# Kernel tuning notes

Measured on AMD Instinct MI355X. Metric: run time of the kernel, lower is better.

## Reference

```python
import jax, jax.numpy as jnp
import numpy as np

B, S, D, H = 2, 2048, 768, 12
DK = D // H
NEG = -10000.0


def setup_inputs() -> dict:
    key = jax.random.key(0)
    ks = jax.random.split(key, 12)
    def lin(k):
        kw, kb = jax.random.split(k)
        return (jax.random.normal(kw, (D, D), jnp.float32) * 0.02,
                jax.random.normal(kb, (D,), jnp.float32) * 0.02)
    Wq, bq = lin(ks[0]); Wk, bk = lin(ks[1]); Wv, bv = lin(ks[2]); Wo, bo = lin(ks[3])
    query = jax.random.normal(ks[4], (B, S, D), jnp.float32)
    key_t = jax.random.normal(ks[5], (B, S, D), jnp.float32)
    value = jax.random.normal(ks[6], (B, S, D), jnp.float32)
    # causal mask, broadcastable to [B,H,S,S]; positions with 0 are masked
    mask = jnp.tril(jnp.ones((S, S), jnp.int32))[None, None, :, :]
    return {"query": query, "key": key_t, "value": value, "mask": mask,
            "Wq": Wq, "bq": bq, "Wk": Wk, "bk": bk, "Wv": Wv, "bv": bv,
            "Wo": Wo, "bo": bo}


def reference(query, key, value, mask, Wq, bq, Wk, bk, Wv, bv, Wo, bo):
    # torch.nn.Linear: y = x @ W^T + b
    def split_heads(x):  # [B,S,D] -> [B,H,S,DK]
        return x.reshape(B, S, H, DK).transpose(0, 2, 1, 3)
    q = split_heads(query @ Wq.T + bq)
    k = split_heads(key @ Wk.T + bk)
    v = split_heads(value @ Wv.T + bv)
    scores = jnp.einsum('bhqd,bhkd->bhqk', q, k) / jnp.sqrt(jnp.float32(DK))
    scores = jnp.where(mask == 0, NEG, scores)  # masked_fill(mask==0, -1e4)
    attn = jax.nn.softmax(scores, axis=-1)      # dropout p=0.0 -> identity
    x = jnp.einsum('bhqk,bhkd->bhqd', attn, v)  # [B,H,S,DK]
    x = x.transpose(0, 2, 1, 3).reshape(B, S, D)
    return x @ Wo.T + bo
```

## Files before the change

### kernel.cpp

```cpp
#include <hip/hip_runtime.h>
#include <cstdint>


#define B_ 2
#define S_ 2048
#define D_ 768
#define H_ 12
#define DK_ 64

typedef __bf16 bf16;
typedef __bf16 bf16x8 __attribute__((ext_vector_type(8)));
typedef float f32x4 __attribute__((ext_vector_type(4)));
typedef uint32_t u32x4 __attribute__((ext_vector_type(4)));
typedef uint16_t u16x4 __attribute__((ext_vector_type(4)));

__device__ __forceinline__ f32x4 mfma16(bf16x8 a, bf16x8 b, f32x4 c) {
  return __builtin_amdgcn_mfma_f32_16x16x32_bf16(a, b, c, 0, 0, 0);
}

struct raw8 { u32x4 a, b; };

__device__ __forceinline__ raw8 fetch8(const void* base, size_t off, int isbf) {
  raw8 r;
  if (isbf) {
    r.a = *(const u32x4*)((const bf16*)base + off);
  } else {
    const float* f = (const float*)base + off;
    r.a = *(const u32x4*)f;
    r.b = *(const u32x4*)(f + 4);
  }
  return r;
}

__device__ __forceinline__ bf16x8 cvt8(raw8 r, int isbf) {
  if (isbf) return __builtin_bit_cast(bf16x8, r.a);
  const float4 x = __builtin_bit_cast(float4, r.a);
  const float4 y = __builtin_bit_cast(float4, r.b);
  bf16x8 o;
  o[0]=(bf16)x.x; o[1]=(bf16)x.y; o[2]=(bf16)x.z; o[3]=(bf16)x.w;
  o[4]=(bf16)y.x; o[5]=(bf16)y.y; o[6]=(bf16)y.z; o[7]=(bf16)y.w;
  return o;
}

__device__ __forceinline__ float load_scalar(const void* base, int idx, int isbf) {
  return isbf ? (float)((const bf16*)base)[idx] : ((const float*)base)[idx];
}

__device__ __forceinline__ uint32_t pack2bf(float lo, float hi) {
  const uint16_t l = __builtin_bit_cast(uint16_t, (bf16)lo);
  const uint16_t h = __builtin_bit_cast(uint16_t, (bf16)hi);
  return (uint32_t)l | ((uint32_t)h << 16);
}

__device__ __forceinline__ int sniff(const void* q) {
  __shared__ int cnt;
  if (threadIdx.x == 0) cnt = 0;
  __syncthreads();
  int local = 0;
  const uint32_t* qw = (const uint32_t*)q;
  for (int i = (int)threadIdx.x; i < 1024; i += 256) {
    const uint32_t e = (qw[i] >> 7) & 0xff;
    if (e >= 96 && e <= 140) local++;
  }
  atomicAdd(&cnt, local);
  __syncthreads();
  return (cnt >= 600) ? 1 : 0;
}

#define GEMM_CVT(Xg, xbf, Wg, wbf, m0, n0)                                   \
  __shared__ __align__(16) bf16 As[2][128][40];                              \
  __shared__ __align__(16) bf16 Bs[2][128][40];                              \
  const int t = (int)threadIdx.x;                                            \
  const int lane = t & 63, w = t >> 6, c = lane & 15, quad = lane >> 4;      \
  const int wm = w & 1, wn = w >> 1;                                         \
  const int srow = t >> 1, scol = (t & 1) * 16;                              \
  f32x4 acc[4][4];                                                           \
  _Pragma("unroll") for (int i = 0; i < 4; ++i)                              \
      _Pragma("unroll") for (int j = 0; j < 4; ++j)                          \
          _Pragma("unroll") for (int e = 0; e < 4; ++e) acc[i][j][e] = 0.0f; \
  raw8 pa[2], pb[2];                                                         \
  auto fetchAB = [&](int k0) {                                               \
    _Pragma("unroll") for (int u = 0; u < 2; ++u) {                          \
      pa[u] = fetch8(Xg, (size_t)(m0 + srow) * D_ + k0 + scol + u * 8, xbf); \
      pb[u] = fetch8(Wg, (size_t)(n0 + srow) * D_ + k0 + scol + u * 8, wbf); \
    }                                                                        \
  };                                                                         \
  fetchAB(0);                                                                \
  int p = 0;                                                                 \
  for (int kt = 0; kt < D_ / 32; ++kt) {                                     \
    _Pragma("unroll") for (int u = 0; u < 2; ++u) {                          \
      *(bf16x8*)&As[p][srow][scol + u * 8] = cvt8(pa[u], xbf);               \
      *(bf16x8*)&Bs[p][srow][scol + u * 8] = cvt8(pb[u], wbf);               \
    }                                                                        \
    __syncthreads();                                                         \
    if (kt + 1 < D_ / 32) fetchAB((kt + 1) * 32);                            \
    bf16x8 af[4], bfr[4];                                                    \
    _Pragma("unroll") for (int i = 0; i < 4; ++i) {                          \
      af[i] = *(const bf16x8*)&As[p][wm * 64 + i * 16 + c][quad * 8];        \
      bfr[i] = *(const bf16x8*)&Bs[p][wn * 64 + i * 16 + c][quad * 8];       \
    }                                                                        \
    _Pragma("unroll") for (int i = 0; i < 4; ++i)                            \
        _Pragma("unroll") for (int j = 0; j < 4; ++j)                        \
            acc[i][j] = mfma16(af[i], bfr[j], acc[i][j]);                    \
    p ^= 1;                                                                  \
  }

__global__ __launch_bounds__(256) void qkv_kernel(
    const void* __restrict__ q, const void* __restrict__ k,
    const void* __restrict__ v,
    const void* __restrict__ Wq, const void* __restrict__ Wk,
    const void* __restrict__ Wv,
    const void* __restrict__ bq, const void* __restrict__ bk,
    const void* __restrict__ bv,
    bf16* __restrict__ qh, bf16* __restrict__ kh, bf16* __restrict__ vt,
    int* __restrict__ flag)
{
  const int isbf = sniff(q);
  if (blockIdx.x == 0 && blockIdx.y == 0 && threadIdx.x == 0) *flag = isbf;
  const int z = (int)blockIdx.y / 6;
  const int n0 = ((int)blockIdx.y % 6) * 128;
  const int m0 = (int)blockIdx.x * 128;
  const void* Xg = (z == 0) ? q : (z == 1) ? k : v;
  const void* Wg = (z == 0) ? Wq : (z == 1) ? Wk : Wv;
  const void* bias = (z == 0) ? bq : (z == 1) ? bk : bv;
  bf16* out = (z == 0) ? qh : (z == 1) ? kh : vt;

  GEMM_CVT(Xg, isbf, Wg, isbf, m0, n0)

#pragma unroll
  for (int j = 0; j < 4; ++j) {
    const int n = n0 + wn * 64 + j * 16 + c;
    const int h = n >> 6, dk = n & 63;
    const float bv_ = load_scalar(bias, n, isbf);
    if (z != 2) {
#pragma unroll
      for (int i = 0; i < 4; ++i)
#pragma unroll
        for (int r = 0; r < 4; ++r) {
          const int m = m0 + wm * 64 + i * 16 + quad * 4 + r;
          const int bi = m >> 11, s = m & (S_ - 1);
          out[(((size_t)bi * H_ + h) * S_ + s) * DK_ + dk] =
              (bf16)(acc[i][j][r] + bv_);
        }
    } else {
#pragma unroll
      for (int i = 0; i < 4; ++i) {
        const int m = m0 + wm * 64 + i * 16 + quad * 4;
        const int bi = m >> 11, s0 = m & (S_ - 1);
        u16x4 pk;
#pragma unroll
        for (int r = 0; r < 4; ++r)
          pk[r] = __builtin_bit_cast(uint16_t, (bf16)(acc[i][j][r] + bv_));
        *(u16x4*)&out[(((size_t)bi * H_ + h) * DK_ + dk) * S_ + s0] = pk;
      }
    }
  }
}

__global__ __launch_bounds__(256) void oproj_kernel(
    const bf16* __restrict__ xh, const void* __restrict__ Wo,
    const void* __restrict__ bias, void* __restrict__ out,
    const int* __restrict__ flag)
{
  const int isbf = *flag;
  const int m0 = (int)blockIdx.x * 128;
  const int n0 = (int)blockIdx.y * 128;

  GEMM_CVT(xh, 1, Wo, isbf, m0, n0)

#pragma unroll
  for (int j = 0; j < 4; ++j) {
    const int n = n0 + wn * 64 + j * 16 + c;
    const float bv_ = load_scalar(bias, n, isbf);
#pragma unroll
    for (int i = 0; i < 4; ++i)
#pragma unroll
      for (int r = 0; r < 4; ++r) {
        const int m = m0 + wm * 64 + i * 16 + quad * 4 + r;
        const float v = acc[i][j][r] + bv_;
        if (isbf) ((bf16*)out)[(size_t)m * D_ + n] = (bf16)v;
        else      ((float*)out)[(size_t)m * D_ + n] = v;
      }
  }
}

__global__ __launch_bounds__(256) void attn_kernel(
    const bf16* __restrict__ qh, const bf16* __restrict__ kh,
    const bf16* __restrict__ vt, bf16* __restrict__ xh)
{
  __shared__ __align__(16) bf16 Ks[2][64][72];
  __shared__ __align__(16) bf16 Vts[2][64][72];

  const int lb = (int)blockIdx.x;
  const int slot = lb >> 8, idx = lb & 255;
  const int i_ = (slot == 0) ? idx : (slot == 1) ? (511 - idx) : (512 + idx);
  const int jt = 31 - i_ / 24;
  const int bh = i_ % 24;
  const int qb = jt * 64;
  const int bi = bh / H_, h = bh % H_;
  const bf16* qp = qh + (size_t)bh * S_ * DK_;
  const bf16* kp = kh + (size_t)bh * S_ * DK_;
  const bf16* vp = vt + (size_t)bh * DK_ * S_;

  const int t = (int)threadIdx.x;
  const int lane = t & 63, w = t >> 6, c = lane & 15, quad = lane >> 4;
  const int r8 = t >> 3, sg = t & 7;
  const float SCL = 0.125f * 1.44269504088896f;

  bf16x8 qB0 = *(const bf16x8*)(qp + (size_t)(qb + w * 16 + c) * DK_ + quad * 8);
  bf16x8 qB1 = *(const bf16x8*)(qp + (size_t)(qb + w * 16 + c) * DK_ + 32 + quad * 8);
#pragma unroll
  for (int i = 0; i < 8; ++i) {
    qB0[i] = (bf16)((float)qB0[i] * SCL);
    qB1[i] = (bf16)((float)qB1[i] * SCL);
  }

  f32x4 accT[4];
#pragma unroll
  for (int nb = 0; nb < 4; ++nb)
#pragma unroll
    for (int i = 0; i < 4; ++i) accT[nb][i] = 0.0f;
  float lp = 0.0f;

  bf16x8 kr0, kr1, vr0, vr1;
  auto loadKV = [&](int kb) {
    kr0 = *(const bf16x8*)(kp + (size_t)(kb + r8) * DK_ + sg * 8);
    kr1 = *(const bf16x8*)(kp + (size_t)(kb + 32 + r8) * DK_ + sg * 8);
    vr0 = *(const bf16x8*)(vp + (size_t)r8 * S_ + kb + sg * 8);
    vr1 = *(const bf16x8*)(vp + (size_t)(r8 + 32) * S_ + kb + sg * 8);
  };

  const int nkt = jt + 1;
  loadKV(0);
  int p = 0;

  for (int kt = 0; kt < nkt; ++kt) {
    *(bf16x8*)&Ks[p][r8][sg * 8]       = kr0;
    *(bf16x8*)&Ks[p][32 + r8][sg * 8]  = kr1;
    *(bf16x8*)&Vts[p][r8][sg * 8]      = vr0;
    *(bf16x8*)&Vts[p][32 + r8][sg * 8] = vr1;
    __syncthreads();
    if (kt + 1 < nkt) loadKV((kt + 1) * 64);
    const bool diag = (kt == nkt - 1);

#pragma unroll
    for (int gq = 0; gq < 2; ++gq) {
      float sv[2][4];
#pragma unroll
      for (int tt = 0; tt < 2; ++tt) {
        const int kl = gq * 32 + tt * 16;
        f32x4 st;
#pragma unroll
        for (int i = 0; i < 4; ++i) st[i] = 0.0f;
        const bf16x8 ka0 = *(const bf16x8*)&Ks[p][kl + c][quad * 8];
        const bf16x8 ka1 = *(const bf16x8*)&Ks[p][kl + c][32 + quad * 8];
        st = mfma16(ka0, qB0, st);
        st = mfma16(ka1, qB1, st);
        if (diag) {
#pragma unroll
          for (int r = 0; r < 4; ++r)
            if (kl + quad * 4 + r > w * 16 + c) st[r] = -__builtin_inff();
        }
#pragma unroll
        for (int r = 0; r < 4; ++r) sv[tt][r] = exp2f(st[r]);
        lp += (sv[tt][0] + sv[tt][1]) + (sv[tt][2] + sv[tt][3]);
      }
      const uint32_t p00 = pack2bf(sv[0][0], sv[0][1]);
      const uint32_t p01 = pack2bf(sv[0][2], sv[0][3]);
      const uint32_t p10 = pack2bf(sv[1][0], sv[1][1]);
      const uint32_t p11 = pack2bf(sv[1][2], sv[1][3]);
      const int aLo = (32 * (quad & 1) + c) * 4;
      const int aHi = aLo + 64;
      const bool tt0 = (quad < 2);
      u32x4 bu;
      {
        const uint32_t t0 = (uint32_t)__builtin_amdgcn_ds_bpermute(aLo, (int)p00);
        const uint32_t t1 = (uint32_t)__builtin_amdgcn_ds_bpermute(aLo, (int)p10);
        bu[0] = tt0 ? t0 : t1;
        const uint32_t t2 = (uint32_t)__builtin_amdgcn_ds_bpermute(aLo, (int)p01);
        const uint32_t t3 = (uint32_t)__builtin_amdgcn_ds_bpermute(aLo, (int)p11);
        bu[1] = tt0 ? t2 : t3;
        const uint32_t t4 = (uint32_t)__builtin_amdgcn_ds_bpermute(aHi, (int)p00);
        const uint32_t t5 = (uint32_t)__builtin_amdgcn_ds_bpermute(aHi, (int)p10);
        bu[2] = tt0 ? t4 : t5;
        const uint32_t t6 = (uint32_t)__builtin_amdgcn_ds_bpermute(aHi, (int)p01);
        const uint32_t t7 = (uint32_t)__builtin_amdgcn_ds_bpermute(aHi, (int)p11);
        bu[3] = tt0 ? t6 : t7;
      }
      const bf16x8 pfrag = __builtin_bit_cast(bf16x8, bu);
#pragma unroll
      for (int nb = 0; nb < 4; ++nb) {
        const bf16x8 vf = *(const bf16x8*)&Vts[p][nb * 16 + c][gq * 32 + quad * 8];
        accT[nb] = mfma16(vf, pfrag, accT[nb]);
      }
    }
    p ^= 1;
  }

  float l = lp;
  l += __shfl_xor(l, 16);
  l += __shfl_xor(l, 32);
  const float inv = 1.0f / l;
  const int s = qb + w * 16 + c;
  bf16* xr = xh + ((size_t)bi * S_ + s) * D_ + h * DK_;
#pragma unroll
  for (int nb = 0; nb < 4; ++nb) {
    u16x4 pk;
#pragma unroll
    for (int r = 0; r < 4; ++r)
      pk[r] = __builtin_bit_cast(uint16_t, (bf16)(accT[nb][r] * inv));
    *(u16x4*)&xr[nb * 16 + quad * 4] = pk;
  }
}

extern "C" void kernel_launch(void* const* d_in, const int* in_sizes, int n_in,
                              void* d_out, int out_size, void* d_ws, size_t ws_size,
                              hipStream_t stream) {
  const void* query = d_in[0];
  const void* key_  = d_in[1];
  const void* value = d_in[2];
  const void* Wq = d_in[4];
  const void* bq = d_in[5];
  const void* Wk = d_in[6];
  const void* bk = d_in[7];
  const void* Wv = d_in[8];
  const void* bv = d_in[9];
  const void* Wo = d_in[10];
  const void* bo = d_in[11];

  const size_t NE = (size_t)B_ * H_ * S_ * DK_;
  bf16* qh  = (bf16*)d_ws;
  bf16* kh  = qh + NE;
  bf16* vt  = kh + NE;
  bf16* xh  = vt + NE;
  int* flag = (int*)(xh + NE);

  dim3 blk(256);
  qkv_kernel<<<dim3(32, 18), blk, 0, stream>>>(
      query, key_, value, Wq, Wk, Wv, bq, bk, bv, qh, kh, vt, flag);
  attn_kernel<<<dim3(768), blk, 0, stream>>>(qh, kh, vt, xh);
  oproj_kernel<<<dim3(32, 6), blk, 0, stream>>>(xh, Wo, bo, d_out, flag);
}
```

Before: 227.9 us.

## Deepen GEMM global prefetch to two stages and swizzle LDS tiles

The projection GEMM macro now keeps two register prefetch stages, issuing global loads two k-tiles ahead so there is more time to hide memory latency. The padded 40-column LDS layout is replaced by a compact 32-column XOR-swizzled layout, which is meant to avoid bank conflicts without padding. This costs extra registers for the second prefetch buffer, which may lower occupancy.

```diff
diff --git a/kernel.cpp b/kernel.cpp
--- a/kernel.cpp
+++ b/kernel.cpp
@@ -50,6 +50,10 @@
   const uint16_t l = __builtin_bit_cast(uint16_t, (bf16)lo);
   const uint16_t h = __builtin_bit_cast(uint16_t, (bf16)hi);
   return (uint32_t)l | ((uint32_t)h << 16);
+}
+
+__device__ __forceinline__ int swz(int row, int col8) {
+  return (row << 5) + (((col8 ^ (row >> 1)) & 3) << 3);
 }
 
 __device__ __forceinline__ int sniff(const void* q) {
@@ -67,42 +71,62 @@
   return (cnt >= 600) ? 1 : 0;
 }
 
+#define GSTEP(KT, PA, PB)                                                    \
+  _Pragma("unroll") for (int u = 0; u < 2; ++u) {                            \
+    *(bf16x8*)&As[p][swz(srow, sc8 + u)] = cvt8(PA[u], xbf_);                \
+    *(bf16x8*)&Bs[p][swz(srow, sc8 + u)] = cvt8(PB[u], wbf_);                \
+  }                                                                          \
+  __syncthreads();                                                           \
+  if ((KT) + 2 < D_ / 32) {                                                  \
+    _Pragma("unroll") for (int u = 0; u < 2; ++u) {                          \
+      PA[u] = fetch8(Xgp, (size_t)(m0_ + srow) * D_ + ((KT) + 2) * 32 +      \
+                              (sc8 + u) * 8, xbf_);                          \
+      PB[u] = fetch8(Wgp, (size_t)(n0_ + srow) * D_ + ((KT) + 2) * 32 +      \
+                              (sc8 + u) * 8, wbf_);                          \
+    }                                                                        \
+  }                                                                          \
+  {                                                                          \
+    bf16x8 af[4], bfr[4];                                                    \
+    _Pragma("unroll") for (int i = 0; i < 4; ++i) {                          \
+      af[i]  = *(const bf16x8*)&As[p][swz(wm * 64 + i * 16 + c, quad)];      \
+      bfr[i] = *(const bf16x8*)&Bs[p][swz(wn * 64 + i * 16 + c, quad)];      \
+    }                                                                        \
+    _Pragma("unroll") for (int i = 0; i < 4; ++i)                            \
+        _Pragma("unroll") for (int j = 0; j < 4; ++j)                        \
+            acc[i][j] = mfma16(af[i], bfr[j], acc[i][j]);                    \
+  }                                                                          \
+  p ^= 1;
+
 #define GEMM_CVT(Xg, xbf, Wg, wbf, m0, n0)                                   \
-  __shared__ __align__(16) bf16 As[2][128][40];                              \
-  __shared__ __align__(16) bf16 Bs[2][128][40];                              \
+  __shared__ __align__(16) bf16 As[2][128 * 32];                             \
+  __shared__ __align__(16) bf16 Bs[2][128 * 32];                             \
+  const void* Xgp = (const void*)(Xg);                                       \
+  const void* Wgp = (const void*)(Wg);                                       \
+  const int xbf_ = (xbf), wbf_ = (wbf);                                      \
+  const int m0_ = (m0), n0_ = (n0);                                          \
   const int t = (int)threadIdx.x;                                            \
   const int lane = t & 63, w = t >> 6, c = lane & 15, quad = lane >> 4;      \
   const int wm = w & 1, wn = w >> 1;                                         \
-  const int srow = t >> 1, scol = (t & 1) * 16;                              \
+  const int srow = t >> 1, sc8 = (t & 1) * 2;                                \
   f32x4 acc[4][4];                                                           \
   _Pragma("unroll") for (int i = 0; i < 4; ++i)                              \
       _Pragma("unroll") for (int j = 0; j < 4; ++j)                          \
           _Pragma("unroll") for (int e = 0; e < 4; ++e) acc[i][j][e] = 0.0f; \
-  raw8 pa[2], pb[2];                                                         \
-  auto fetchAB = [&](int k0) {                                               \
-    _Pragma("unroll") for (int u = 0; u < 2; ++u) {                          \
-      pa[u] = fetch8(Xg, (size_t)(m0 + srow) * D_ + k0 + scol + u * 8, xbf); \
-      pb[u] = fetch8(Wg, (size_t)(n0 + srow) * D_ + k0 + scol + u * 8, wbf); \
-    }                                                                        \
-  };                                                                         \
-  fetchAB(0);                                                                \
+  raw8 pa0[2], pb0[2], pa1[2], pb1[2];                                       \
+  _Pragma("unroll") for (int u = 0; u < 2; ++u) {                            \
+    pa0[u] = fetch8(Xgp, (size_t)(m0_ + srow) * D_ + (sc8 + u) * 8, xbf_);   \
+    pb0[u] = fetch8(Wgp, (size_t)(n0_ + srow) * D_ + (sc8 + u) * 8, wbf_);   \
+  }                                                                          \
+  _Pragma("unroll") for (int u = 0; u < 2; ++u) {                            \
+    pa1[u] = fetch8(Xgp, (size_t)(m0_ + srow) * D_ + 32 + (sc8 + u) * 8,     \
+                    xbf_);                                                   \
+    pb1[u] = fetch8(Wgp, (size_t)(n0_ + srow) * D_ + 32 + (sc8 + u) * 8,     \
+                    wbf_);                                                   \
+  }                                                                          \
   int p = 0;                                                                 \
-  for (int kt = 0; kt < D_ / 32; ++kt) {                                     \
-    _Pragma("unroll") for (int u = 0; u < 2; ++u) {                          \
-      *(bf16x8*)&As[p][srow][scol + u * 8] = cvt8(pa[u], xbf);               \
-      *(bf16x8*)&Bs[p][srow][scol + u * 8] = cvt8(pb[u], wbf);               \
-    }                                                                        \
-    __syncthreads();                                                         \
-    if (kt + 1 < D_ / 32) fetchAB((kt + 1) * 32);                            \
-    bf16x8 af[4], bfr[4];                                                    \
-    _Pragma("unroll") for (int i = 0; i < 4; ++i) {                          \
-      af[i] = *(const bf16x8*)&As[p][wm * 64 + i * 16 + c][quad * 8];        \
-      bfr[i] = *(const bf16x8*)&Bs[p][wn * 64 + i * 16 + c][quad * 8];       \
-    }                                                                        \
-    _Pragma("unroll") for (int i = 0; i < 4; ++i)                            \
-        _Pragma("unroll") for (int j = 0; j < 4; ++j)                        \
-            acc[i][j] = mfma16(af[i], bfr[j], acc[i][j]);                    \
-    p ^= 1;                                                                  \
+  for (int kt = 0; kt < D_ / 32; kt += 2) {                                  \
+    GSTEP(kt, pa0, pb0)                                                      \
+    GSTEP(kt + 1, pa1, pb1)                                                  \
   }
 
 __global__ __launch_bounds__(256) void qkv_kernel(
```

After: 240.1 us. 5.4% more time.

## Load GEMM MFMA fragments directly from global memory instead of LDS staging

Applied to the files above, without the earlier changes.

Drops the double-buffered shared-memory tiles in the QKV and output projection GEMMs. Each wave now loads its bf16x8 MFMA fragments straight from global memory, converting from fp32 where needed, which removes the LDS writes, the block barriers and the shared-memory footprint. In exchange, tiles are no longer shared between waves, so each A/B fragment is fetched twice by different waves. The 16-byte-per-lane loads are also strided by whole rows, which relies on L1/L2 hits and may expose global latency without the prefetch overlap.

```diff
diff --git a/kernel.cpp b/kernel.cpp
--- a/kernel.cpp
+++ b/kernel.cpp
@@ -18,24 +18,11 @@
   return __builtin_amdgcn_mfma_f32_16x16x32_bf16(a, b, c, 0, 0, 0);
 }
 
-struct raw8 { u32x4 a, b; };
-
-__device__ __forceinline__ raw8 fetch8(const void* base, size_t off, int isbf) {
-  raw8 r;
-  if (isbf) {
-    r.a = *(const u32x4*)((const bf16*)base + off);
-  } else {
-    const float* f = (const float*)base + off;
-    r.a = *(const u32x4*)f;
-    r.b = *(const u32x4*)(f + 4);
-  }
-  return r;
-}
-
-__device__ __forceinline__ bf16x8 cvt8(raw8 r, int isbf) {
-  if (isbf) return __builtin_bit_cast(bf16x8, r.a);
-  const float4 x = __builtin_bit_cast(float4, r.a);
-  const float4 y = __builtin_bit_cast(float4, r.b);
+__device__ __forceinline__ bf16x8 ldfrag(const void* base, size_t off, int isbf) {
+  if (isbf) return *(const bf16x8*)((const bf16*)base + off);
+  const float* f = (const float*)base + off;
+  const float4 x = *(const float4*)f;
+  const float4 y = *(const float4*)(f + 4);
   bf16x8 o;
   o[0]=(bf16)x.x; o[1]=(bf16)x.y; o[2]=(bf16)x.z; o[3]=(bf16)x.w;
   o[4]=(bf16)y.x; o[5]=(bf16)y.y; o[6]=(bf16)y.z; o[7]=(bf16)y.w;
@@ -67,42 +54,29 @@
   return (cnt >= 600) ? 1 : 0;
 }
 
-#define GEMM_CVT(Xg, xbf, Wg, wbf, m0, n0)                                   \
-  __shared__ __align__(16) bf16 As[2][128][40];                              \
-  __shared__ __align__(16) bf16 Bs[2][128][40];                              \
+#define GEMM_DIRECT(Xg, xbf, Wg, wbf, m0, n0)                                \
   const int t = (int)threadIdx.x;                                            \
   const int lane = t & 63, w = t >> 6, c = lane & 15, quad = lane >> 4;      \
   const int wm = w & 1, wn = w >> 1;                                         \
-  const int srow = t >> 1, scol = (t & 1) * 16;                              \
   f32x4 acc[4][4];                                                           \
   _Pragma("unroll") for (int i = 0; i < 4; ++i)                              \
       _Pragma("unroll") for (int j = 0; j < 4; ++j)                          \
           _Pragma("unroll") for (int e = 0; e < 4; ++e) acc[i][j][e] = 0.0f; \
-  raw8 pa[2], pb[2];                                                         \
-  auto fetchAB = [&](int k0) {                                               \
-    _Pragma("unroll") for (int u = 0; u < 2; ++u) {                          \
-      pa[u] = fetch8(Xg, (size_t)(m0 + srow) * D_ + k0 + scol + u * 8, xbf); \
-      pb[u] = fetch8(Wg, (size_t)(n0 + srow) * D_ + k0 + scol + u * 8, wbf); \
-    }                                                                        \
-  };                                                                         \
-  fetchAB(0);                                                                \
-  int p = 0;                                                                 \
-  for (int kt = 0; kt < D_ / 32; ++kt) {                                     \
-    _Pragma("unroll") for (int u = 0; u < 2; ++u) {                          \
-      *(bf16x8*)&As[p][srow][scol + u * 8] = cvt8(pa[u], xbf);               \
-      *(bf16x8*)&Bs[p][srow][scol + u * 8] = cvt8(pb[u], wbf);               \
-    }                                                                        \
-    __syncthreads();                                                         \
-    if (kt + 1 < D_ / 32) fetchAB((kt + 1) * 32);                            \
+  size_t aoff[4], boff[4];                                                   \
+  _Pragma("unroll") for (int i = 0; i < 4; ++i) {                            \
+    aoff[i] = (size_t)((m0) + wm * 64 + i * 16 + c) * D_ + quad * 8;         \
+    boff[i] = (size_t)((n0) + wn * 64 + i * 16 + c) * D_ + quad * 8;         \
+  }                                                                          \
+  _Pragma("unroll 2") for (int kt = 0; kt < D_ / 32; ++kt) {                 \
+    const int k0 = kt * 32;                                                  \
     bf16x8 af[4], bfr[4];                                                    \
-    _Pragma("unroll") for (int i = 0; i < 4; ++i) {                          \
-      af[i] = *(const bf16x8*)&As[p][wm * 64 + i * 16 + c][quad * 8];        \
-      bfr[i] = *(const bf16x8*)&Bs[p][wn * 64 + i * 16 + c][quad * 8];       \
-    }                                                                        \
+    _Pragma("unroll") for (int i = 0; i < 4; ++i)                            \
+      af[i] = ldfrag(Xg, aoff[i] + k0, xbf);                                 \
+    _Pragma("unroll") for (int j = 0; j < 4; ++j)                            \
+      bfr[j] = ldfrag(Wg, boff[j] + k0, wbf);                                \
     _Pragma("unroll") for (int i = 0; i < 4; ++i)                            \
         _Pragma("unroll") for (int j = 0; j < 4; ++j)                        \
             acc[i][j] = mfma16(af[i], bfr[j], acc[i][j]);                    \
-    p ^= 1;                                                                  \
   }
 
 __global__ __launch_bounds__(256) void qkv_kernel(
@@ -125,7 +99,7 @@
   const void* bias = (z == 0) ? bq : (z == 1) ? bk : bv;
   bf16* out = (z == 0) ? qh : (z == 1) ? kh : vt;
 
-  GEMM_CVT(Xg, isbf, Wg, isbf, m0, n0)
+  GEMM_DIRECT(Xg, isbf, Wg, isbf, m0, n0)
 
 #pragma unroll
   for (int j = 0; j < 4; ++j) {
@@ -166,7 +140,7 @@
   const int m0 = (int)blockIdx.x * 128;
   const int n0 = (int)blockIdx.y * 128;
 
-  GEMM_CVT(xh, 1, Wo, isbf, m0, n0)
+  GEMM_DIRECT(xh, 1, Wo, isbf, m0, n0)
 
 #pragma unroll
   for (int j = 0; j < 4; ++j) {
```

New measurement: 371.9 us. 63.2% more time.
